# Optimization experiments

Hardware: AMD Instinct MI355X
Metric: run time of the kernel (lower is better)

Reference implementation:

```python
import jax, jax.numpy as jnp
import numpy as np

QMIN, QMAX = -128, 127  # 8-bit signed quantized range


def setup_inputs() -> dict:
    key = jax.random.key(0)
    k0, k1, k2, k3 = jax.random.split(key, 4)
    N, Cin, H, W = 64, 128, 56, 56
    Cout, K = 128, 3
    x = jax.random.randint(k0, (N, Cin, H, W), -128, 128, dtype=jnp.int32).astype(jnp.int8)
    weight = jax.random.randint(k1, (Cout, Cin, K, K), -128, 128, dtype=jnp.int32).astype(jnp.int8)
    # int32 bias (already shifted by -Zx*sum(W) in the original quantization flow)
    bias = jax.random.randint(k2, (Cout,), -4096, 4096, dtype=jnp.int32)
    input_scale = jnp.float32(0.02)
    weight_scale = jax.random.uniform(k3, (Cout,), minval=0.001, maxval=0.01, dtype=jnp.float32)  # per-channel
    output_scale = jnp.float32(0.05)
    input_zero_point = -3   # python int, constant
    output_zero_point = -2  # python int, constant
    return {"x": x, "weight": weight, "bias": bias,
            "input_scale": input_scale, "weight_scale": weight_scale,
            "output_scale": output_scale,
            "input_zero_point": input_zero_point,
            "output_zero_point": output_zero_point}


def reference(x, weight, bias, input_scale, weight_scale, output_scale,
              input_zero_point, output_zero_point):
    # pad spatial dims with the INPUT zero point (padding=(1,1), as in the torch module)
    xp = jnp.pad(x, ((0, 0), (0, 0), (1, 1), (1, 1)), constant_values=input_zero_point)
    acc = jax.lax.conv_general_dilated(
        xp.astype(jnp.int32), weight.astype(jnp.int32),
        window_strides=(1, 1), padding='VALID',
        rhs_dilation=(1, 1), dimension_numbers=('NCHW', 'OIHW', 'NCHW'))
    acc = acc + bias[None, :, None, None]                       # [N,Co,Ho,Wo] int32
    # requantize: per-output-channel scale, shift by output zero point
    scale = (input_scale * weight_scale / output_scale)[None, :, None, None]
    out = acc.astype(jnp.float32) * scale + jnp.float32(output_zero_point)
    return jnp.clip(jnp.round(out), QMIN, QMAX).astype(jnp.int8)
```

## Files before the change

### kernel.cpp

```cpp
#include <hip/hip_runtime.h>


#define CIN  128
#define COUT 128
#define HW   56
#define NPIX (HW * HW)
#define ROWS  2
#define QCOLS 58
#define XROW  (QCOLS * CIN)
#define XP_OFF 147456
#define XP_ROWS (64 * QCOLS)

typedef int v4i  __attribute__((ext_vector_type(4)));
typedef int v16i __attribute__((ext_vector_type(16)));

__device__ __forceinline__ void gl16(const void* g, void* l) {
    __builtin_amdgcn_global_load_lds(
        (const __attribute__((address_space(1))) unsigned*)g,
        (__attribute__((address_space(3))) unsigned*)l, 16, 0, 0);
}

__global__ __launch_bounds__(256) void pack_w2(const int* __restrict__ w_g,
                                               unsigned* __restrict__ wp2) {
    int i = blockIdx.x * 256 + threadIdx.x;
    if (i >= 36 * 128 * 8) return;
    int dw   = i & 7;
    int cout = (i >> 3) & 127;
    int step = i >> 10;
    int t  = step >> 2;
    int cb = step & 3;
    unsigned d = 0;
#pragma unroll
    for (int b = 0; b < 4; ++b) {
        int ci = cb * 32 + dw * 4 + b;
        int v = w_g[(cout * CIN + ci) * 9 + t];
        d |= (unsigned)(v & 0xFF) << (8 * b);
    }
    int g  = (cout << 1) | (dw >> 2);
    int gs = g ^ ((g >> 3) & 7);
    wp2[step * 1024 + gs * 4 + (dw & 3)] = d;
}

#define LSTR 57
__global__ __launch_bounds__(256) void repack_x(const int* __restrict__ x_g,
                                                unsigned char* __restrict__ xp,
                                                const int* __restrict__ zp_in_p) {
    __shared__ int lx[CIN * LSTR];
    const int blk = blockIdx.x;
    const int n  = blk / QCOLS;
    const int hp = blk % QCOLS;
    const int tid = threadIdx.x;
    const unsigned zpd = (unsigned)((*zp_in_p) & 0xFF) * 0x01010101u;
    unsigned* row = (unsigned*)(xp + (size_t)blk * XROW);

    if (hp == 0 || hp == QCOLS - 1) {
#pragma unroll
        for (int it = 0; it < 8; ++it) {
            int d = it * 256 + tid;
            if (d < QCOLS * 32) row[d] = zpd;
        }
        return;
    }
    const int h = hp - 1;
    const int* xrow = x_g + (n * CIN * HW + h) * HW;
#pragma unroll
    for (int it = 0; it < 7; ++it) {
        int idx = it * 256 + tid;
        int ci  = idx / 14;
        int w4  = (idx - ci * 14) * 4;
        v4i L = *(const v4i*)(xrow + ci * NPIX + w4);
        int* ld = &lx[ci * LSTR + w4];
        ld[0] = L[0]; ld[1] = L[1]; ld[2] = L[2]; ld[3] = L[3];
    }
    __syncthreads();
#pragma unroll
    for (int it = 0; it < 8; ++it) {
        int d = it * 256 + tid;
        if (d < QCOLS * 32) {
            int wp  = d >> 5;
            int ci4 = d & 31;
            unsigned v = zpd;
            if (wp >= 1 && wp <= HW) {
                const int* lb = &lx[ci4 * 4 * LSTR + (wp - 1)];
                v = (unsigned)(lb[0] & 0xFF) |
                    ((unsigned)(lb[LSTR] & 0xFF) << 8) |
                    ((unsigned)(lb[2 * LSTR] & 0xFF) << 16) |
                    ((unsigned)(lb[3 * LSTR] & 0xFF) << 24);
            }
            row[d] = v;
        }
    }
}

__global__ __launch_bounds__(256, 4) void conv_mfma(
    const unsigned char* __restrict__ xp, const unsigned char* __restrict__ wp2b,
    const int* __restrict__ bias, const float* __restrict__ in_s,
    const float* __restrict__ w_s, const float* __restrict__ out_s,
    const int* __restrict__ zp_out_p, int* __restrict__ out) {
    __shared__ unsigned char xsb[29696];
    __shared__ float scs[COUT];
    __shared__ float ofs[COUT];

    const int n   = blockIdx.x / 28;
    const int ho0 = (blockIdx.x % 28) * ROWS;
    const int tid    = threadIdx.x;
    const int lane   = tid & 63;
    const int wave   = tid >> 6;
    const int lane31 = lane & 31;
    const int hi     = lane >> 5;
    const int hi4    = hi * 4;

    if (tid < COUT) {
        float sc = ((*in_s) / (*out_s)) * w_s[tid];
        scs[tid] = sc;
        ofs[tid] = (float)bias[tid] * sc + (float)(*zp_out_p);
    }

    const unsigned char* win = xp + (size_t)(n * QCOLS + ho0) * XROW;
    const int qrel = lane >> 3;
    const int lof  = (qrel * 8 + ((lane & 7) ^ qrel)) * 16;
    for (int i = wave; i < 29; i += 4)
        gl16(win + i * 1024 + lof, xsb + i * 1024);
    __syncthreads();

    const unsigned* xs = (const unsigned*)xsb;
    const int px  = wave * 32 + lane31;
    const int pxc = px < ROWS * HW ? px : ROWS * HW - 1;
    const int qb  = (pxc / HW) * QCOLS + (pxc % HW);
    int bo0, bo1, bo2, bo3;
    {
        int g0 = 0 * 64 + lane31 * 2 + hi;
        int g1 = 1 * 64 + lane31 * 2 + hi;
        int g2 = 2 * 64 + lane31 * 2 + hi;
        int g3 = 3 * 64 + lane31 * 2 + hi;
        bo0 = (g0 ^ ((g0 >> 3) & 7)) * 16;
        bo1 = (g1 ^ ((g1 >> 3) & 7)) * 16;
        bo2 = (g2 ^ ((g2 >> 3) & 7)) * 16;
        bo3 = (g3 ^ ((g3 >> 3) & 7)) * 16;
    }

    v16i acc0 = (v16i)0, acc1 = (v16i)0, acc2 = (v16i)0, acc3 = (v16i)0;

#define LOADB(B0, B1, B2, B3, S)                                             \
    {                                                                        \
        const int so = (S) * 4096;                                           \
        B0 = *(const v4i*)(wp2b + so + bo0);                                 \
        B1 = *(const v4i*)(wp2b + so + bo1);                                 \
        B2 = *(const v4i*)(wp2b + so + bo2);                                 \
        B3 = *(const v4i*)(wp2b + so + bo3);                                 \
    }
#define LDA(AF, S)                                                           \
    {                                                                        \
        const int t  = (S) >> 2;                                             \
        const int kr = (t * 11) >> 5;                                        \
        const int q  = qb + kr * QCOLS + (t - 3 * kr);                       \
        const int cb = (S) & 3;                                              \
        AF = *(const v4i*)&xs[q * 32 + ((cb * 8 + hi4) ^ ((q & 7) << 2))];   \
    }
#define FIRE(AF, B0, B1, B2, B3)                                             \
    {                                                                        \
        acc0 = __builtin_amdgcn_mfma_i32_32x32x32_i8(B0, AF, acc0, 0, 0, 0); \
        acc1 = __builtin_amdgcn_mfma_i32_32x32x32_i8(B1, AF, acc1, 0, 0, 0); \
        acc2 = __builtin_amdgcn_mfma_i32_32x32x32_i8(B2, AF, acc2, 0, 0, 0); \
        acc3 = __builtin_amdgcn_mfma_i32_32x32x32_i8(B3, AF, acc3, 0, 0, 0); \
    }

    v4i aA, aB, bA0, bA1, bA2, bA3, bB0, bB1, bB2, bB3;
    LOADB(bA0, bA1, bA2, bA3, 0); LDA(aA, 0);
    LOADB(bB0, bB1, bB2, bB3, 1); LDA(aB, 1);
#pragma unroll 1
    for (int ss = 0; ss < 36; ss += 2) {
        FIRE(aA, bA0, bA1, bA2, bA3);
        if (ss + 2 < 36) { LOADB(bA0, bA1, bA2, bA3, ss + 2); LDA(aA, ss + 2); }
        FIRE(aB, bB0, bB1, bB2, bB3);
        if (ss + 3 < 36) { LOADB(bB0, bB1, bB2, bB3, ss + 3); LDA(aB, ss + 3); }
    }
#undef FIRE
#undef LDA
#undef LOADB

    if (px < ROWS * HW) {
        int* ob = out + n * COUT * NPIX + ho0 * HW + px;
        const v16i* accs[1];
#pragma unroll
        for (int nt = 0; nt < 4; ++nt) {
            const v16i& A = (nt == 0) ? acc0 : (nt == 1) ? acc1 : (nt == 2) ? acc2 : acc3;
#pragma unroll
            for (int reg = 0; reg < 16; ++reg) {
                int co = nt * 32 + (reg & 3) + 8 * (reg >> 2) + hi4;
                float f = fmaf((float)A[reg], scs[co], ofs[co]);
                f = rintf(f);
                f = fminf(fmaxf(f, -128.0f), 127.0f);
                ob[co * NPIX] = (int)f;
            }
        }
        (void)accs;
    }
}

extern "C" void kernel_launch(void* const* d_in, const int* in_sizes, int n_in,
                              void* d_out, int out_size, void* d_ws, size_t ws_size,
                              hipStream_t stream) {
    const int* x_g      = (const int*)d_in[0];
    const int* w_g      = (const int*)d_in[1];
    const int* bias     = (const int*)d_in[2];
    const float* in_s   = (const float*)d_in[3];
    const float* w_s    = (const float*)d_in[4];
    const float* out_s  = (const float*)d_in[5];
    const int* zp_in_p  = (const int*)d_in[6];
    const int* zp_out_p = (const int*)d_in[7];
    int* outp = (int*)d_out;
    unsigned* wp2 = (unsigned*)d_ws;
    unsigned char* xpp = (unsigned char*)d_ws + XP_OFF;

    pack_w2<<<(36 * 128 * 8 + 255) / 256, 256, 0, stream>>>(w_g, wp2);
    repack_x<<<XP_ROWS, 256, 0, stream>>>(x_g, xpp, zp_in_p);

    const int nblocks = 64 * (HW / ROWS);
    conv_mfma<<<nblocks, 256, 0, stream>>>(xpp, (const unsigned char*)wp2, bias,
                                           in_s, w_s, out_s, zp_out_p, outp);
}
```

Baseline: 88.92 us.

## Enlarge conv tile to four rows with 2x2 wave MFMA sub-tiling

The conv block now covers four output rows with 512 threads, and each of 8 waves computes a 64-pixel by 64-channel sub-tile (2x2 MFMAs) instead of 32 pixels by all 128 channels. This halves the weight fragment loads per MFMA and improves reuse of the input halo rows staged in LDS. In exchange it uses more LDS per block, halves the block count, and duplicates A loads across the two channel-halves.

```diff
diff --git a/kernel.cpp b/kernel.cpp
--- a/kernel.cpp
+++ b/kernel.cpp
@@ -5,7 +5,7 @@
 #define COUT 128
 #define HW   56
 #define NPIX (HW * HW)
-#define ROWS  2
+#define ROWS  4
 #define QCOLS 58
 #define XROW  (QCOLS * CIN)
 #define XP_OFF 147456
@@ -92,20 +92,22 @@
     }
 }
 
-__global__ __launch_bounds__(256, 4) void conv_mfma(
+__global__ __launch_bounds__(512, 4) void conv_mfma(
     const unsigned char* __restrict__ xp, const unsigned char* __restrict__ wp2b,
     const int* __restrict__ bias, const float* __restrict__ in_s,
     const float* __restrict__ w_s, const float* __restrict__ out_s,
     const int* __restrict__ zp_out_p, int* __restrict__ out) {
-    __shared__ unsigned char xsb[29696];
+    __shared__ unsigned char xsb[45056];
     __shared__ float scs[COUT];
     __shared__ float ofs[COUT];
 
-    const int n   = blockIdx.x / 28;
-    const int ho0 = (blockIdx.x % 28) * ROWS;
+    const int n   = blockIdx.x / 14;
+    const int ho0 = (blockIdx.x % 14) * ROWS;
     const int tid    = threadIdx.x;
     const int lane   = tid & 63;
     const int wave   = tid >> 6;
+    const int mp     = wave & 3;
+    const int np     = wave >> 2;
     const int lane31 = lane & 31;
     const int hi     = lane >> 5;
     const int hi4    = hi * 4;
@@ -119,82 +121,88 @@
     const unsigned char* win = xp + (size_t)(n * QCOLS + ho0) * XROW;
     const int qrel = lane >> 3;
     const int lof  = (qrel * 8 + ((lane & 7) ^ qrel)) * 16;
-    for (int i = wave; i < 29; i += 4)
-        gl16(win + i * 1024 + lof, xsb + i * 1024);
+    for (int i = wave; i < 44; i += 8) {
+        int off = i * 1024 + lof;
+        if (i == 43 && qrel >= 4) off = 0;
+        gl16(win + off, xsb + i * 1024);
+    }
     __syncthreads();
 
     const unsigned* xs = (const unsigned*)xsb;
-    const int px  = wave * 32 + lane31;
-    const int pxc = px < ROWS * HW ? px : ROWS * HW - 1;
-    const int qb  = (pxc / HW) * QCOLS + (pxc % HW);
-    int bo0, bo1, bo2, bo3;
+    const int px0 = mp * 64 + lane31;
+    const int px1 = mp * 64 + 32 + lane31;
+    const int px1c = px1 < ROWS * HW ? px1 : ROWS * HW - 1;
+    const int qb0 = (px0 / HW) * QCOLS + (px0 % HW);
+    const int qb1 = (px1c / HW) * QCOLS + (px1c % HW);
+    int bo0, bo1;
     {
-        int g0 = 0 * 64 + lane31 * 2 + hi;
-        int g1 = 1 * 64 + lane31 * 2 + hi;
-        int g2 = 2 * 64 + lane31 * 2 + hi;
-        int g3 = 3 * 64 + lane31 * 2 + hi;
+        int g0 = (np * 2 + 0) * 64 + lane31 * 2 + hi;
+        int g1 = (np * 2 + 1) * 64 + lane31 * 2 + hi;
         bo0 = (g0 ^ ((g0 >> 3) & 7)) * 16;
         bo1 = (g1 ^ ((g1 >> 3) & 7)) * 16;
-        bo2 = (g2 ^ ((g2 >> 3) & 7)) * 16;
-        bo3 = (g3 ^ ((g3 >> 3) & 7)) * 16;
-    }
-
-    v16i acc0 = (v16i)0, acc1 = (v16i)0, acc2 = (v16i)0, acc3 = (v16i)0;
-
-#define LOADB(B0, B1, B2, B3, S)                                             \
+    }
+
+    v16i acc00 = (v16i)0, acc01 = (v16i)0, acc10 = (v16i)0, acc11 = (v16i)0;
+
+#define LOADB(B0, B1, S)                                                     \
     {                                                                        \
         const int so = (S) * 4096;                                           \
         B0 = *(const v4i*)(wp2b + so + bo0);                                 \
         B1 = *(const v4i*)(wp2b + so + bo1);                                 \
-        B2 = *(const v4i*)(wp2b + so + bo2);                                 \
-        B3 = *(const v4i*)(wp2b + so + bo3);                                 \
-    }
-#define LDA(AF, S)                                                           \
+    }
+#define LDA(A0, A1, S)                                                       \
     {                                                                        \
         const int t  = (S) >> 2;                                             \
         const int kr = (t * 11) >> 5;                                        \
-        const int q  = qb + kr * QCOLS + (t - 3 * kr);                       \
+        const int dq = kr * QCOLS + (t - 3 * kr);                            \
+        const int q0 = qb0 + dq, q1 = qb1 + dq;                              \
         const int cb = (S) & 3;                                              \
-        AF = *(const v4i*)&xs[q * 32 + ((cb * 8 + hi4) ^ ((q & 7) << 2))];   \
-    }
-#define FIRE(AF, B0, B1, B2, B3)                                             \
+        A0 = *(const v4i*)&xs[q0 * 32 + ((cb * 8 + hi4) ^ ((q0 & 7) << 2))]; \
+        A1 = *(const v4i*)&xs[q1 * 32 + ((cb * 8 + hi4) ^ ((q1 & 7) << 2))]; \
+    }
+#define FIRE(A0, A1, B0, B1)                                                 \
     {                                                                        \
-        acc0 = __builtin_amdgcn_mfma_i32_32x32x32_i8(B0, AF, acc0, 0, 0, 0); \
-        acc1 = __builtin_amdgcn_mfma_i32_32x32x32_i8(B1, AF, acc1, 0, 0, 0); \
-        acc2 = __builtin_amdgcn_mfma_i32_32x32x32_i8(B2, AF, acc2, 0, 0, 0); \
-        acc3 = __builtin_amdgcn_mfma_i32_32x32x32_i8(B3, AF, acc3, 0, 0, 0); \
-    }
-
-    v4i aA, aB, bA0, bA1, bA2, bA3, bB0, bB1, bB2, bB3;
-    LOADB(bA0, bA1, bA2, bA3, 0); LDA(aA, 0);
-    LOADB(bB0, bB1, bB2, bB3, 1); LDA(aB, 1);
+        acc00 = __builtin_amdgcn_mfma_i32_32x32x32_i8(B0, A0, acc00, 0, 0, 0); \
+        acc01 = __builtin_amdgcn_mfma_i32_32x32x32_i8(B1, A0, acc01, 0, 0, 0); \
+        acc10 = __builtin_amdgcn_mfma_i32_32x32x32_i8(B0, A1, acc10, 0, 0, 0); \
+        acc11 = __builtin_amdgcn_mfma_i32_32x32x32_i8(B1, A1, acc11, 0, 0, 0); \
+    }
+
+    v4i aA0, aA1, aB0, aB1, bA0, bA1, bB0, bB1;
+    LOADB(bA0, bA1, 0); LDA(aA0, aA1, 0);
+    LOADB(bB0, bB1, 1); LDA(aB0, aB1, 1);
 #pragma unroll 1
     for (int ss = 0; ss < 36; ss += 2) {
-        FIRE(aA, bA0, bA1, bA2, bA3);
-        if (ss + 2 < 36) { LOADB(bA0, bA1, bA2, bA3, ss + 2); LDA(aA, ss + 2); }
-        FIRE(aB, bB0, bB1, bB2, bB3);
-        if (ss + 3 < 36) { LOADB(bB0, bB1, bB2, bB3, ss + 3); LDA(aB, ss + 3); }
+        FIRE(aA0, aA1, bA0, bA1);
+        if (ss + 2 < 36) { LOADB(bA0, bA1, ss + 2); LDA(aA0, aA1, ss + 2); }
+        FIRE(aB0, aB1, bB0, bB1);
+        if (ss + 3 < 36) { LOADB(bB0, bB1, ss + 3); LDA(aB0, aB1, ss + 3); }
     }
 #undef FIRE
 #undef LDA
 #undef LOADB
 
-    if (px < ROWS * HW) {
-        int* ob = out + n * COUT * NPIX + ho0 * HW + px;
-        const v16i* accs[1];
-#pragma unroll
-        for (int nt = 0; nt < 4; ++nt) {
-            const v16i& A = (nt == 0) ? acc0 : (nt == 1) ? acc1 : (nt == 2) ? acc2 : acc3;
-#pragma unroll
-            for (int reg = 0; reg < 16; ++reg) {
-                int co = nt * 32 + (reg & 3) + 8 * (reg >> 2) + hi4;
-                float f = fmaf((float)A[reg], scs[co], ofs[co]);
-                f = rintf(f);
-                f = fminf(fmaxf(f, -128.0f), 127.0f);
-                ob[co * NPIX] = (int)f;
+    const int obase = n * COUT * NPIX + ho0 * HW;
+#pragma unroll
+    for (int mi = 0; mi < 2; ++mi) {
+        const int px = mp * 64 + mi * 32 + lane31;
+        if (px < ROWS * HW) {
+            int* ob = out + obase + px;
+#pragma unroll
+            for (int ni = 0; ni < 2; ++ni) {
+                const v16i& A = (mi == 0) ? (ni == 0 ? acc00 : acc01)
+                                          : (ni == 0 ? acc10 : acc11);
+                const int ntb = (np * 2 + ni) * 32;
+#pragma unroll
+                for (int reg = 0; reg < 16; ++reg) {
+                    int co = ntb + (reg & 3) + 8 * (reg >> 2) + hi4;
+                    float f = fmaf((float)A[reg], scs[co], ofs[co]);
+                    f = rintf(f);
+                    f = fminf(fmaxf(f, -128.0f), 127.0f);
+                    ob[co * NPIX] = (int)f;
+                }
             }
         }
-        (void)accs;
     }
 }
 
@@ -217,6 +225,6 @@
     repack_x<<<XP_ROWS, 256, 0, stream>>>(x_g, xpp, zp_in_p);
 
     const int nblocks = 64 * (HW / ROWS);
-    conv_mfma<<<nblocks, 256, 0, stream>>>(xpp, (const unsigned char*)wp2, bias,
+    conv_mfma<<<nblocks, 512, 0, stream>>>(xpp, (const unsigned char*)wp2, bias,
                                            in_s, w_s, out_s, zp_out_p, outp);
 }
```

Measured after the change: 84.05 us. 1.06x faster.
